# Optimization experiments

Hardware: AMD Instinct MI355X
Metric: run time of the kernel (lower is better)

Reference implementation:

```python
import jax, jax.numpy as jnp
import numpy as np

N_NODES = 4096
IN_FEAT = 256
N_HEADS = 8
N_HIDDEN = 32  # out_features // n_heads
NEG_SLOPE = 0.2


def setup_inputs() -> dict:
    key = jax.random.key(0)
    k1, k2, k3, k4 = jax.random.split(key, 4)
    h = jax.random.normal(k1, (N_NODES, IN_FEAT), dtype=jnp.float32)
    W = jax.random.normal(k2, (N_HEADS * N_HIDDEN, IN_FEAT), dtype=jnp.float32) * 0.05
    a = jax.random.normal(k3, (2 * N_HIDDEN,), dtype=jnp.float32) * 0.05
    adj_mat = jax.random.randint(k4, (N_NODES, N_NODES, 1), 0, 2, dtype=jnp.int32)
    return {"h": h, "W": W, "a": a, "adj_mat": adj_mat}


def reference(h, W, a, adj_mat):
    n = h.shape[0]
    # g = linear(h) -> [N, H, F]
    g = (h @ W.T).reshape(n, N_HEADS, N_HIDDEN)
    # e_ij = LeakyReLU(a^T [g_i || g_j]) = LeakyReLU(a_l . g_i + a_r . g_j)
    a_l, a_r = a[:N_HIDDEN], a[N_HIDDEN:]
    s_i = jnp.einsum('nhf,f->nh', g, a_l)  # destination term (repeat_interleave axis)
    s_j = jnp.einsum('nhf,f->nh', g, a_r)  # source term (repeat axis)
    e = jax.nn.leaky_relu(s_i[:, None, :] + s_j[None, :, :], NEG_SLOPE)  # [N, N, H]
    e = jnp.where(adj_mat == 0, jnp.float32(-jnp.inf), e)
    att = jax.nn.softmax(e, axis=1)  # softmax over source nodes j
    # dropout(p) in eval mode -> identity
    out = jnp.einsum('ijh,jhf->ihf', att, g)
    return out.reshape(n, N_HEADS * N_HIDDEN)  # is_concat=True
```

## Files before the change

### kernel.cpp

```cpp
#include <hip/hip_runtime.h>
#include <math.h>

constexpr int N   = 4096;
constexpr int F   = 256;
constexpr int NH  = 8;
constexpr int HID = 32;
constexpr float SLOPE = 0.2f;

using h2       = __attribute__((ext_vector_type(2))) _Float16;
using frag_f16 = __attribute__((ext_vector_type(8))) _Float16;
using frag_cd  = __attribute__((ext_vector_type(4))) float;
using frag_c16 = __attribute__((ext_vector_type(16))) float;

__device__ inline unsigned short f2h(float x) {
  _Float16 v = (_Float16)x;
  unsigned short u; __builtin_memcpy(&u, &v, 2); return u;
}

__global__ __launch_bounds__(256) void k_u(const float* __restrict__ W,
                                           const float* __restrict__ a,
                                           float* __restrict__ U) {
  const int c = blockIdx.x, k = threadIdx.x;
  const int head = c & 7, side = c >> 3;
  float acc = 0.f;
#pragma unroll
  for (int f = 0; f < 32; ++f)
    acc += W[(size_t)(head * 32 + f) * F + k] * a[side * 32 + f];
  U[c * F + k] = acc;
}

__global__ __launch_bounds__(256) void k_front(const float* __restrict__ h,
                                               const float* __restrict__ W,
                                               const float* __restrict__ U,
                                               const int* __restrict__ adj,
                                               unsigned int* __restrict__ RT2,
                                               unsigned short* __restrict__ BT,
                                               unsigned short* __restrict__ DT,
                                               unsigned short* __restrict__ gT,
                                               unsigned int* __restrict__ bits) {
  const int b = blockIdx.x, t = threadIdx.x;
  if (b < 256) {
    const int i0 = b * 16;
    const int r = t >> 4, c = t & 15;
    const float4* hp = (const float4*)(h + (size_t)(i0 + r) * F);
    const float4* up = (const float4*)(U + (size_t)c * F);
    float acc = 0.f;
#pragma unroll
    for (int k4 = 0; k4 < 64; ++k4) {
      const float4 hv = hp[k4];
      const float4 uv = up[k4];
      acc += hv.x * uv.x + hv.y * uv.y + hv.z * uv.z + hv.w * uv.w;
    }
    const int n = i0 + r;
    if (c < 8) {
      const unsigned int r16 = f2h(__expf(-0.8f * acc));
      RT2[(size_t)n * NH + c] = (r16 << 16) | r16;
    } else {
      const int hd = c - 8;
      BT[(size_t)hd * N + n] = f2h(__expf(acc));
      DT[(size_t)hd * N + n] = f2h(__expf(SLOPE * acc));
    }
  } else if (b < 1280) {
    const int lane = t & 63;
    const int tile = (b - 256) * 4 + (t >> 6);
    const int mt = tile >> 4, nt = tile & 15;
    const int m0 = mt * 16, n0 = nt * 16;
    const int n16 = lane & 15, quad = lane >> 4;
    frag_cd acc = {0.f, 0.f, 0.f, 0.f};
    const float* ap = h + (size_t)(m0 + n16) * F + quad * 8;
    const float* bp = W + (size_t)(n0 + n16) * F + quad * 8;
#pragma unroll
    for (int ks = 0; ks < F / 32; ++ks) {
      const float4 a0 = *(const float4*)(ap + ks * 32);
      const float4 a1 = *(const float4*)(ap + ks * 32 + 4);
      const float4 b0 = *(const float4*)(bp + ks * 32);
      const float4 b1 = *(const float4*)(bp + ks * 32 + 4);
      const frag_f16 af = {(_Float16)a0.x, (_Float16)a0.y, (_Float16)a0.z, (_Float16)a0.w,
                           (_Float16)a1.x, (_Float16)a1.y, (_Float16)a1.z, (_Float16)a1.w};
      const frag_f16 bf = {(_Float16)b0.x, (_Float16)b0.y, (_Float16)b0.z, (_Float16)b0.w,
                           (_Float16)b1.x, (_Float16)b1.y, (_Float16)b1.z, (_Float16)b1.w};
      acc = __builtin_amdgcn_mfma_f32_16x16x32_f16(af, bf, acc, 0, 0, 0);
    }
    unsigned short tmp[4];
#pragma unroll
    for (int reg = 0; reg < 4; ++reg) tmp[reg] = f2h(acc[reg]);
    *(int2*)(gT + (size_t)(n0 + n16) * N + m0 + quad * 4) = *(int2*)tmp;
  } else {
    const int lane = t & 63;
    const int wv   = t >> 6;
    const int row  = (b - 1280) * 2 + (wv >> 1);
    const int half = wv & 1;
    const int4* src4 = (const int4*)(adj + (size_t)row * N) + half * 512 + lane;
    const int shamt = (lane & 7) * 4;
    unsigned int* dstw = bits + (size_t)row * (N / 32) + half * 64 + (lane >> 3);
#pragma unroll
    for (int it = 0; it < 8; ++it) {
      const int4 v4 = src4[it * 64];
      unsigned int v = ((unsigned)v4.x | ((unsigned)v4.y << 1) |
                        ((unsigned)v4.z << 2) | ((unsigned)v4.w << 3)) << shamt;
      v |= (unsigned)__shfl_xor((int)v, 1);
      v |= (unsigned)__shfl_xor((int)v, 2);
      v |= (unsigned)__shfl_xor((int)v, 4);
      if ((lane & 7) == 0) dstw[it * 8] = v;
    }
  }
}

constexpr int TI = 64;
constexpr int NSPLIT = 4;

__global__ __launch_bounds__(256, 4) void k_agg(
    const unsigned short* __restrict__ gT,
    const unsigned int* __restrict__ RT2,
    const unsigned short* __restrict__ BT, const unsigned short* __restrict__ DT,
    const unsigned int* __restrict__ bits,
    float* __restrict__ parts, float* __restrict__ lparts) {
  __shared__ __align__(16) unsigned short sB[64][140];
  __shared__ __align__(16) uint4 sBD[2][2][128];

  const int t    = threadIdx.x;
  const int lane = t & 63;
  const int wv   = t >> 6;
  const int isub = wv & 1;
  const int hd   = wv >> 1;
  const int b    = blockIdx.x;
  const int hp   = b & 3;
  const int js   = (b >> 2) & (NSPLIT - 1);
  const int i0   = (b >> 4) * TI;
  const int head = hp * 2 + hd;

  const int n32 = lane & 31;
  const int kh  = lane >> 5;

  const int myi = i0 + isub * 32 + n32;
  const unsigned int Ri2u = RT2[(size_t)myi * NH + head];
  h2 Ri2; __builtin_memcpy(&Ri2, &Ri2u, 4);
  const uint4* bp4 = (const uint4*)(bits + (size_t)myi * (N / 32) + js * 32);

  frag_c16 acc = {0.f, 0.f, 0.f, 0.f, 0.f, 0.f, 0.f, 0.f,
                  0.f, 0.f, 0.f, 0.f, 0.f, 0.f, 0.f, 0.f};
  frag_c16 accl = {0.f, 0.f, 0.f, 0.f, 0.f, 0.f, 0.f, 0.f,
                   0.f, 0.f, 0.f, 0.f, 0.f, 0.f, 0.f, 0.f};
  frag_f16 fone;
#pragma unroll
  for (int u = 0; u < 8; ++u) fone[u] = (_Float16)1.0f;

  const int sr = t >> 2, ss0 = t & 3;
  const unsigned short* gsrc = gT + (size_t)(hp * 64 + sr) * N + js * 1024;

  {
    const int hsel = t >> 7, idx = t & 127;
    sBD[0][hsel][idx] =
        ((const uint4*)(BT + (size_t)(hp * 2 + hsel) * N + js * 1024))[idx];
    sBD[1][hsel][idx] =
        ((const uint4*)(DT + (size_t)(hp * 2 + hsel) * N + js * 1024))[idx];
  }
  {
    int4 pre[4];
#pragma unroll
    for (int s = 0; s < 4; ++s)
      pre[s] = *(const int4*)(gsrc + (ss0 + s * 4) * 8);
#pragma unroll
    for (int s = 0; s < 4; ++s) {
      const int seg = ss0 + s * 4;
      *(int2*)&sB[sr][seg * 8]     = make_int2(pre[s].x, pre[s].y);
      *(int2*)&sB[sr][seg * 8 + 4] = make_int2(pre[s].z, pre[s].w);
    }
  }
  __syncthreads();

  for (int c8 = 0; c8 < 8; ++c8) {
    int4 nxt[4];
    if (c8 < 7) {
#pragma unroll
      for (int s = 0; s < 4; ++s)
        nxt[s] = *(const int4*)(gsrc + (c8 + 1) * 128 + (ss0 + s * 4) * 8);
    }
    const uint4 bw = bp4[c8];
    const unsigned int bwa[4] = {bw.x, bw.y, bw.z, bw.w};
#pragma unroll
    for (int ss = 0; ss < 8; ++ss) {
      const int jb = ss * 16 + kh * 8;
      const uint4 Bv = sBD[0][hd][c8 * 16 + ss * 2 + kh];
      const uint4 Dv = sBD[1][hd][c8 * 16 + ss * 2 + kh];
      const unsigned int mb = (bwa[ss >> 1] >> (((ss & 1) << 4) + (kh << 3))) & 0xFFu;
      const unsigned int bu[4] = {Bv.x, Bv.y, Bv.z, Bv.w};
      const unsigned int du[4] = {Dv.x, Dv.y, Dv.z, Dv.w};
      unsigned int packed[4];
#pragma unroll
      for (int p = 0; p < 4; ++p) {
        h2 hB, hD;
        __builtin_memcpy(&hB, &bu[p], 4);
        __builtin_memcpy(&hD, &du[p], 4);
        const h2 wm = __builtin_elementwise_max(hB, Ri2 * hD);
        unsigned int wp; __builtin_memcpy(&wp, &wm, 4);
        const unsigned int d  = (mb >> (2 * p)) & 3u;
        const unsigned int sp = ((d | (d << 15)) & 0x10001u) * 0xFFFFu;
        wp &= sp;
        packed[p] = wp;
      }
      frag_f16 af; __builtin_memcpy(&af, packed, 16);

      const int frow = hd * 32 + n32;
      const int2 blo = *(const int2*)&sB[frow][jb];
      const int2 bhi = *(const int2*)&sB[frow][jb + 4];
      const int bt[4] = {blo.x, blo.y, bhi.x, bhi.y};
      frag_f16 bf; __builtin_memcpy(&bf, bt, 16);

      acc  = __builtin_amdgcn_mfma_f32_32x32x16_f16(af, bf, acc, 0, 0, 0);
      accl = __builtin_amdgcn_mfma_f32_32x32x16_f16(af, fone, accl, 0, 0, 0);
    }
    if (c8 < 7) {
      __syncthreads();
#pragma unroll
      for (int s = 0; s < 4; ++s) {
        const int seg = ss0 + s * 4;
        *(int2*)&sB[sr][seg * 8]     = make_int2(nxt[s].x, nxt[s].y);
        *(int2*)&sB[sr][seg * 8 + 4] = make_int2(nxt[s].z, nxt[s].w);
      }
      __syncthreads();
    }
  }

  float* op = parts + (size_t)js * N * F;
#pragma unroll
  for (int reg = 0; reg < 16; ++reg) {
    const int row = (reg & 3) + 8 * (reg >> 2) + 4 * kh;
    op[(size_t)(i0 + isub * 32 + row) * F + head * HID + n32] = acc[reg];
  }
  if (n32 == 0) {
    float* lp = lparts + (size_t)js * N * NH;
#pragma unroll
    for (int reg = 0; reg < 16; ++reg) {
      const int row = (reg & 3) + 8 * (reg >> 2) + 4 * kh;
      lp[(size_t)(i0 + isub * 32 + row) * NH + head] = accl[reg];
    }
  }
}

__global__ __launch_bounds__(256) void k_norm(const float* __restrict__ parts,
                                              const float* __restrict__ lparts,
                                              float* __restrict__ out) {
  const int idx = blockIdx.x * 256 + threadIdx.x;
  const int i = idx >> 6, fq = idx & 63;
  const int hh = fq >> 3;
  float l = 0.f;
  float4 v = make_float4(0.f, 0.f, 0.f, 0.f);
#pragma unroll
  for (int js = 0; js < NSPLIT; ++js) {
    l += lparts[(size_t)js * N * NH + (size_t)i * NH + hh];
    const float4 p = *(const float4*)(parts + (size_t)js * N * F + (size_t)idx * 4);
    v.x += p.x; v.y += p.y; v.z += p.z; v.w += p.w;
  }
  const float inv = 1.f / l;
  v.x *= inv; v.y *= inv; v.z *= inv; v.w *= inv;
  *(float4*)(out + (size_t)idx * 4) = v;
}

extern "C" void kernel_launch(void* const* d_in, const int* in_sizes, int n_in,
                              void* d_out, int out_size, void* d_ws, size_t ws_size,
                              hipStream_t stream) {
  const float* h   = (const float*)d_in[0];
  const float* W   = (const float*)d_in[1];
  const float* a   = (const float*)d_in[2];
  const int*   adj = (const int*)d_in[3];
  float* out = (float*)d_out;

  char* ws = (char*)d_ws;
  unsigned short* gT = (unsigned short*)ws;  ws += (size_t)N * F * 2;
  unsigned int* bits = (unsigned int*)ws;    ws += (size_t)N * (N / 32) * 4;
  unsigned int* RT2 = (unsigned int*)ws;     ws += (size_t)N * NH * 4;
  unsigned short* BT = (unsigned short*)ws;  ws += (size_t)N * NH * 2;
  unsigned short* DT = (unsigned short*)ws;  ws += (size_t)N * NH * 2;
  float* U    = (float*)ws;                  ws += 16 * F * 4;
  float* parts  = (float*)ws;                ws += (size_t)NSPLIT * N * F * 4;
  float* lparts = (float*)ws;                ws += (size_t)NSPLIT * N * NH * 4;

  k_u<<<dim3(16), dim3(256), 0, stream>>>(W, a, U);
  k_front<<<dim3(3328), dim3(256), 0, stream>>>(h, W, U, adj, RT2, BT, DT, gT, bits);
  k_agg<<<dim3((N / TI) * 4 * NSPLIT), dim3(256), 0, stream>>>(
      gT, RT2, BT, DT, bits, parts, lparts);
  k_norm<<<dim3(N * F / 4 / 256), dim3(256), 0, stream>>>(parts, lparts, out);
}
```

Measured before the change: 157.0 us.

## Split fused front kernel into three launches and XOR-swizzle shared gT tile

Breaks the branchy k_front kernel into separate k_bits, k_sln and k_gemm launches. In k_agg, the padded shared tile (row stride 140) is replaced by an unpadded 128-wide tile with an XOR swizzle on 16-byte segments. This lets the tile be written and read with single 128-bit LDS accesses instead of pairs of 64-bit ones, while aiming to avoid bank conflicts. Splitting the front kernel adds two extra launches and removes the overlap between the three heterogeneous front tasks, but each kernel becomes uniform.

Result: slower. 179.7 us (+14.5%).

```diff
diff --git a/kernel.cpp b/kernel.cpp
--- a/kernel.cpp
+++ b/kernel.cpp
@@ -29,80 +29,83 @@
   U[c * F + k] = acc;
 }
 
-__global__ __launch_bounds__(256) void k_front(const float* __restrict__ h,
-                                               const float* __restrict__ W,
-                                               const float* __restrict__ U,
-                                               const int* __restrict__ adj,
-                                               unsigned int* __restrict__ RT2,
-                                               unsigned short* __restrict__ BT,
-                                               unsigned short* __restrict__ DT,
-                                               unsigned short* __restrict__ gT,
-                                               unsigned int* __restrict__ bits) {
+__global__ __launch_bounds__(256) void k_sln(const float* __restrict__ h,
+                                             const float* __restrict__ U,
+                                             unsigned int* __restrict__ RT2,
+                                             unsigned short* __restrict__ BT,
+                                             unsigned short* __restrict__ DT) {
   const int b = blockIdx.x, t = threadIdx.x;
-  if (b < 256) {
-    const int i0 = b * 16;
-    const int r = t >> 4, c = t & 15;
-    const float4* hp = (const float4*)(h + (size_t)(i0 + r) * F);
-    const float4* up = (const float4*)(U + (size_t)c * F);
-    float acc = 0.f;
-#pragma unroll
-    for (int k4 = 0; k4 < 64; ++k4) {
-      const float4 hv = hp[k4];
-      const float4 uv = up[k4];
-      acc += hv.x * uv.x + hv.y * uv.y + hv.z * uv.z + hv.w * uv.w;
-    }
-    const int n = i0 + r;
-    if (c < 8) {
-      const unsigned int r16 = f2h(__expf(-0.8f * acc));
-      RT2[(size_t)n * NH + c] = (r16 << 16) | r16;
-    } else {
-      const int hd = c - 8;
-      BT[(size_t)hd * N + n] = f2h(__expf(acc));
-      DT[(size_t)hd * N + n] = f2h(__expf(SLOPE * acc));
-    }
-  } else if (b < 1280) {
-    const int lane = t & 63;
-    const int tile = (b - 256) * 4 + (t >> 6);
-    const int mt = tile >> 4, nt = tile & 15;
-    const int m0 = mt * 16, n0 = nt * 16;
-    const int n16 = lane & 15, quad = lane >> 4;
-    frag_cd acc = {0.f, 0.f, 0.f, 0.f};
-    const float* ap = h + (size_t)(m0 + n16) * F + quad * 8;
-    const float* bp = W + (size_t)(n0 + n16) * F + quad * 8;
-#pragma unroll
-    for (int ks = 0; ks < F / 32; ++ks) {
-      const float4 a0 = *(const float4*)(ap + ks * 32);
-      const float4 a1 = *(const float4*)(ap + ks * 32 + 4);
-      const float4 b0 = *(const float4*)(bp + ks * 32);
-      const float4 b1 = *(const float4*)(bp + ks * 32 + 4);
-      const frag_f16 af = {(_Float16)a0.x, (_Float16)a0.y, (_Float16)a0.z, (_Float16)a0.w,
-                           (_Float16)a1.x, (_Float16)a1.y, (_Float16)a1.z, (_Float16)a1.w};
-      const frag_f16 bf = {(_Float16)b0.x, (_Float16)b0.y, (_Float16)b0.z, (_Float16)b0.w,
-                           (_Float16)b1.x, (_Float16)b1.y, (_Float16)b1.z, (_Float16)b1.w};
-      acc = __builtin_amdgcn_mfma_f32_16x16x32_f16(af, bf, acc, 0, 0, 0);
-    }
-    unsigned short tmp[4];
-#pragma unroll
-    for (int reg = 0; reg < 4; ++reg) tmp[reg] = f2h(acc[reg]);
-    *(int2*)(gT + (size_t)(n0 + n16) * N + m0 + quad * 4) = *(int2*)tmp;
+  const int i0 = b * 16;
+  const int r = t >> 4, c = t & 15;
+  const float4* hp = (const float4*)(h + (size_t)(i0 + r) * F);
+  const float4* up = (const float4*)(U + (size_t)c * F);
+  float acc = 0.f;
+#pragma unroll
+  for (int k4 = 0; k4 < 64; ++k4) {
+    const float4 hv = hp[k4];
+    const float4 uv = up[k4];
+    acc += hv.x * uv.x + hv.y * uv.y + hv.z * uv.z + hv.w * uv.w;
+  }
+  const int n = i0 + r;
+  if (c < 8) {
+    const unsigned int r16 = f2h(__expf(-0.8f * acc));
+    RT2[(size_t)n * NH + c] = (r16 << 16) | r16;
   } else {
-    const int lane = t & 63;
-    const int wv   = t >> 6;
-    const int row  = (b - 1280) * 2 + (wv >> 1);
-    const int half = wv & 1;
-    const int4* src4 = (const int4*)(adj + (size_t)row * N) + half * 512 + lane;
-    const int shamt = (lane & 7) * 4;
-    unsigned int* dstw = bits + (size_t)row * (N / 32) + half * 64 + (lane >> 3);
-#pragma unroll
-    for (int it = 0; it < 8; ++it) {
-      const int4 v4 = src4[it * 64];
-      unsigned int v = ((unsigned)v4.x | ((unsigned)v4.y << 1) |
-                        ((unsigned)v4.z << 2) | ((unsigned)v4.w << 3)) << shamt;
-      v |= (unsigned)__shfl_xor((int)v, 1);
-      v |= (unsigned)__shfl_xor((int)v, 2);
-      v |= (unsigned)__shfl_xor((int)v, 4);
-      if ((lane & 7) == 0) dstw[it * 8] = v;
-    }
+    const int hd = c - 8;
+    BT[(size_t)hd * N + n] = f2h(__expf(acc));
+    DT[(size_t)hd * N + n] = f2h(__expf(SLOPE * acc));
+  }
+}
+
+__global__ __launch_bounds__(256) void k_gemm(const float* __restrict__ h,
+                                              const float* __restrict__ W,
+                                              unsigned short* __restrict__ gT) {
+  const int b = blockIdx.x, t = threadIdx.x;
+  const int lane = t & 63;
+  const int tile = b * 4 + (t >> 6);
+  const int mt = tile >> 4, nt = tile & 15;
+  const int m0 = mt * 16, n0 = nt * 16;
+  const int n16 = lane & 15, quad = lane >> 4;
+  frag_cd acc = {0.f, 0.f, 0.f, 0.f};
+  const float* ap = h + (size_t)(m0 + n16) * F + quad * 8;
+  const float* bp = W + (size_t)(n0 + n16) * F + quad * 8;
+#pragma unroll
+  for (int ks = 0; ks < F / 32; ++ks) {
+    const float4 a0 = *(const float4*)(ap + ks * 32);
+    const float4 a1 = *(const float4*)(ap + ks * 32 + 4);
+    const float4 b0 = *(const float4*)(bp + ks * 32);
+    const float4 b1 = *(const float4*)(bp + ks * 32 + 4);
+    const frag_f16 af = {(_Float16)a0.x, (_Float16)a0.y, (_Float16)a0.z, (_Float16)a0.w,
+                         (_Float16)a1.x, (_Float16)a1.y, (_Float16)a1.z, (_Float16)a1.w};
+    const frag_f16 bf = {(_Float16)b0.x, (_Float16)b0.y, (_Float16)b0.z, (_Float16)b0.w,
+                         (_Float16)b1.x, (_Float16)b1.y, (_Float16)b1.z, (_Float16)b1.w};
+    acc = __builtin_amdgcn_mfma_f32_16x16x32_f16(af, bf, acc, 0, 0, 0);
+  }
+  unsigned short tmp[4];
+#pragma unroll
+  for (int reg = 0; reg < 4; ++reg) tmp[reg] = f2h(acc[reg]);
+  *(int2*)(gT + (size_t)(n0 + n16) * N + m0 + quad * 4) = *(int2*)tmp;
+}
+
+__global__ __launch_bounds__(256) void k_bits(const int* __restrict__ adj,
+                                              unsigned int* __restrict__ bits) {
+  const int b = blockIdx.x, t = threadIdx.x;
+  const int lane = t & 63;
+  const int wv   = t >> 6;
+  const int row  = b * 2 + (wv >> 1);
+  const int half = wv & 1;
+  const int4* src4 = (const int4*)(adj + (size_t)row * N) + half * 512 + lane;
+  const int shamt = (lane & 7) * 4;
+  unsigned int* dstw = bits + (size_t)row * (N / 32) + half * 64 + (lane >> 3);
+#pragma unroll
+  for (int it = 0; it < 8; ++it) {
+    const int4 v4 = src4[it * 64];
+    unsigned int v = ((unsigned)v4.x | ((unsigned)v4.y << 1) |
+                      ((unsigned)v4.z << 2) | ((unsigned)v4.w << 3)) << shamt;
+    v |= (unsigned)__shfl_xor((int)v, 1);
+    v |= (unsigned)__shfl_xor((int)v, 2);
+    v |= (unsigned)__shfl_xor((int)v, 4);
+    if ((lane & 7) == 0) dstw[it * 8] = v;
   }
 }
 
@@ -115,7 +118,7 @@
     const unsigned short* __restrict__ BT, const unsigned short* __restrict__ DT,
     const unsigned int* __restrict__ bits,
     float* __restrict__ parts, float* __restrict__ lparts) {
-  __shared__ __align__(16) unsigned short sB[64][140];
+  __shared__ __align__(16) unsigned short sB[64][128];
   __shared__ __align__(16) uint4 sBD[2][2][128];
 
   const int t    = threadIdx.x;
@@ -163,8 +166,7 @@
 #pragma unroll
     for (int s = 0; s < 4; ++s) {
       const int seg = ss0 + s * 4;
-      *(int2*)&sB[sr][seg * 8]     = make_int2(pre[s].x, pre[s].y);
-      *(int2*)&sB[sr][seg * 8 + 4] = make_int2(pre[s].z, pre[s].w);
+      *(int4*)&sB[sr][((seg ^ (sr & 15)) * 8)] = pre[s];
     }
   }
   __syncthreads();
@@ -180,7 +182,6 @@
     const unsigned int bwa[4] = {bw.x, bw.y, bw.z, bw.w};
 #pragma unroll
     for (int ss = 0; ss < 8; ++ss) {
-      const int jb = ss * 16 + kh * 8;
       const uint4 Bv = sBD[0][hd][c8 * 16 + ss * 2 + kh];
       const uint4 Dv = sBD[1][hd][c8 * 16 + ss * 2 + kh];
       const unsigned int mb = (bwa[ss >> 1] >> (((ss & 1) << 4) + (kh << 3))) & 0xFFu;
@@ -202,10 +203,9 @@
       frag_f16 af; __builtin_memcpy(&af, packed, 16);
 
       const int frow = hd * 32 + n32;
-      const int2 blo = *(const int2*)&sB[frow][jb];
-      const int2 bhi = *(const int2*)&sB[frow][jb + 4];
-      const int bt[4] = {blo.x, blo.y, bhi.x, bhi.y};
-      frag_f16 bf; __builtin_memcpy(&bf, bt, 16);
+      const int lg   = ss * 2 + kh;
+      const int4 bv  = *(const int4*)&sB[frow][((lg ^ (frow & 15)) * 8)];
+      frag_f16 bf; __builtin_memcpy(&bf, &bv, 16);
 
       acc  = __builtin_amdgcn_mfma_f32_32x32x16_f16(af, bf, acc, 0, 0, 0);
       accl = __builtin_amdgcn_mfma_f32_32x32x16_f16(af, fone, accl, 0, 0, 0);
@@ -215,8 +215,7 @@
 #pragma unroll
       for (int s = 0; s < 4; ++s) {
         const int seg = ss0 + s * 4;
-        *(int2*)&sB[sr][seg * 8]     = make_int2(nxt[s].x, nxt[s].y);
-        *(int2*)&sB[sr][seg * 8 + 4] = make_int2(nxt[s].z, nxt[s].w);
+        *(int4*)&sB[sr][((seg ^ (sr & 15)) * 8)] = nxt[s];
       }
       __syncthreads();
     }
@@ -277,7 +276,9 @@
   float* lparts = (float*)ws;                ws += (size_t)NSPLIT * N * NH * 4;
 
   k_u<<<dim3(16), dim3(256), 0, stream>>>(W, a, U);
-  k_front<<<dim3(3328), dim3(256), 0, stream>>>(h, W, U, adj, RT2, BT, DT, gT, bits);
+  k_bits<<<dim3(N / 2), dim3(256), 0, stream>>>(adj, bits);
+  k_sln<<<dim3(N / 16), dim3(256), 0, stream>>>(h, U, RT2, BT, DT);
+  k_gemm<<<dim3((N / 16) * (F / 16) / 4, 1, 1), dim3(256), 0, stream>>>(h, W, gT);
   k_agg<<<dim3((N / TI) * 4 * NSPLIT), dim3(256), 0, stream>>>(
       gT, RT2, BT, DT, bits, parts, lparts);
   k_norm<<<dim3(N * F / 4 / 256), dim3(256), 0, stream>>>(parts, lparts, out);
```
